# Kernel optimization log

Hardware: AMD Instinct MI355X
Metric: run time of the kernel (lower is better)

## Reference

```python
import jax, jax.numpy as jnp
import numpy as np

D = 512      # model_dim
H = 8        # num_heads
HD = D // H  # head_dim = 64
S = 196      # tokens per channel (14x14 grid)
CHANNELS = np.array([2, 4, 6, 4], dtype=np.int32)  # multiplex channels per sample


def setup_inputs() -> dict:
    key = jax.random.key(0)
    ks = jax.random.split(key, 8)
    C = int(CHANNELS.sum())  # 16
    n = lambda k, shp, s=1.0: jax.random.normal(k, shp, dtype=jnp.float32) * s
    return {
        "x_query": n(ks[0], (C, S, D)),
        "x_keyval": n(ks[1], (C, S, D)),
        "pos": n(ks[2], (C, S, D)),
        "channels": CHANNELS,
        "Wq": n(ks[3], (D, D), 0.02), "bq": jnp.zeros((D,), jnp.float32),
        "Wk": n(ks[4], (D, D), 0.02), "bk": jnp.zeros((D,), jnp.float32),
        "Wv": n(ks[5], (D, D), 0.02), "bv": jnp.zeros((D,), jnp.float32),
        "Wo": n(ks[6], (D, D), 0.02), "bo": jnp.zeros((D,), jnp.float32),
    }


def reference(x_query, x_keyval, pos, channels, Wq, bq, Wk, bk, Wv, bv, Wo, bo):
    C, S_, D_ = x_query.shape
    ch = np.asarray(channels)
    # segment id per packed token; segment i has length channels[i]*S (== cu_seq_len blocks)
    seg = np.repeat(np.arange(ch.shape[0]), ch * S_)                # [T] static
    block_mask = seg[:, None] == seg[None, :]                        # [T,T] static bool

    xq = x_query.reshape(-1, D_)   # [T,D]
    xk = x_keyval.reshape(-1, D_)
    p = pos.reshape(-1, D_)

    # positional embedding fused into Q/K before projection (query_pos/key_pos)
    q = ((xq + p) @ Wq + bq).reshape(-1, H, HD)
    k = ((xk + p) @ Wk + bk).reshape(-1, H, HD)
    v = (xk @ Wv + bv).reshape(-1, H, HD)

    scale = 1.0 / np.sqrt(HD)
    scores = jnp.einsum('qhd,khd->hqk', q, k) * scale               # [H,T,T]
    scores = jnp.where(block_mask[None], scores, jnp.float32(-1e30))
    attn = jax.nn.softmax(scores, axis=-1)
    out = jnp.einsum('hqk,khd->qhd', attn, v).reshape(-1, D_)       # [T,D]
    out = out @ Wo + bo
    return out.reshape(C, S_, D_)
```

## Files before the change

### kernel.cpp

```cpp
#include <hip/hip_runtime.h>
#include <hip/hip_bf16.h>


typedef short short8 __attribute__((ext_vector_type(8)));
typedef float f32x4 __attribute__((ext_vector_type(4)));

__device__ __forceinline__ float b2f(unsigned short u) {
    union { float f; unsigned int i; } x; x.i = ((unsigned int)u) << 16; return x.f;
}
__device__ __forceinline__ unsigned short f2b(float f) {
    union { float f; unsigned int i; } x; x.f = f;
    unsigned int r = x.i + 0x7fffu + ((x.i >> 16) & 1u);
    return (unsigned short)(r >> 16);
}

#define NE 1605632
#define WE 262144
#define GS 72

__launch_bounds__(256)
__global__ void prep(const float* __restrict__ xq, const float* __restrict__ xk,
                     const float* __restrict__ pos,
                     const float* __restrict__ W0, const float* __restrict__ W1,
                     const float* __restrict__ W2, const float* __restrict__ W3,
                     unsigned short* __restrict__ WF,
                     unsigned short* __restrict__ aqb, unsigned short* __restrict__ akb,
                     unsigned short* __restrict__ xkbb) {
    const int tid = threadIdx.x;
    if (blockIdx.z < 4) {
        if (blockIdx.x >= 128) return;
        const float* W = blockIdx.z == 0 ? W0 : blockIdx.z == 1 ? W1 : blockIdx.z == 2 ? W2 : W3;
        unsigned short* T = WF + (size_t)blockIdx.z * WE;
        const int s = blockIdx.x * 4 + (tid >> 6);
        const int f = s >> 4, t = s & 15;
        const int lane = tid & 63, quad = lane >> 4, l16 = lane & 15;
        short8 o;
        #pragma unroll
        for (int j = 0; j < 8; ++j)
            o[j] = (short)f2b(W[(size_t)(t * 32 + quad * 8 + j) * 512 + f * 16 + l16]);
        *(short8*)(T + (size_t)s * 512 + lane * 8) = o;
    } else {
        const size_t e = ((size_t)blockIdx.x * 256 + tid) * 8;
        f32x4 q0 = *(const f32x4*)(xq + e),  q1 = *(const f32x4*)(xq + e + 4);
        f32x4 k0 = *(const f32x4*)(xk + e),  k1 = *(const f32x4*)(xk + e + 4);
        f32x4 p0 = *(const f32x4*)(pos + e), p1 = *(const f32x4*)(pos + e + 4);
        short8 a, b, c;
        #pragma unroll
        for (int j = 0; j < 4; ++j) {
            a[j] = (short)f2b(q0[j] + p0[j]); a[4 + j] = (short)f2b(q1[j] + p1[j]);
            b[j] = (short)f2b(k0[j] + p0[j]); b[4 + j] = (short)f2b(k1[j] + p1[j]);
            c[j] = (short)f2b(k0[j]);         c[4 + j] = (short)f2b(k1[j]);
        }
        *(short8*)(aqb + e)  = a;
        *(short8*)(akb + e)  = b;
        *(short8*)(xkbb + e) = c;
    }
}

template <bool OUT_F32>
__device__ __forceinline__ void gemm_wave(const unsigned short* __restrict__ A,
                                          const unsigned short* __restrict__ WFw,
                                          const float* __restrict__ bias,
                                          void* __restrict__ C,
                                          int m0, int n0) {
    const int lane = threadIdx.x & 63;
    const int quad = lane >> 4, l16 = lane & 15;
    const int f0 = n0 >> 4;
    const unsigned short* Arow = A + (size_t)(m0 + l16) * 512 + quad * 8;
    const unsigned short* Bbase = WFw + (size_t)lane * 8;

    f32x4 acc[4] = {};
    #pragma unroll 4
    for (int t = 0; t < 16; ++t) {
        short8 af = *(const short8*)(Arow + t * 32);
        #pragma unroll
        for (int nt = 0; nt < 4; ++nt) {
            short8 bf = *(const short8*)(Bbase + (size_t)((f0 + nt) * 16 + t) * 512);
            acc[nt] = __builtin_amdgcn_mfma_f32_16x16x32_bf16(af, bf, acc[nt], 0, 0, 0);
        }
    }
    #pragma unroll
    for (int nt = 0; nt < 4; ++nt) {
        const int col = n0 + nt * 16 + l16;
        const float bv = bias[col];
        #pragma unroll
        for (int r = 0; r < 4; ++r) {
            const int row = m0 + quad * 4 + r;
            float cv = acc[nt][r] + bv;
            if constexpr (OUT_F32) ((float*)C)[(size_t)row * 512 + col] = cv;
            else ((unsigned short*)C)[(size_t)row * 512 + col] = f2b(cv);
        }
    }
}

__launch_bounds__(256)
__global__ void qkv_gemm(const unsigned short* __restrict__ aqb,
                         const unsigned short* __restrict__ akb,
                         const unsigned short* __restrict__ xkbb,
                         const unsigned short* __restrict__ WF,
                         const float* __restrict__ bq, const float* __restrict__ bk,
                         const float* __restrict__ bv,
                         unsigned short* __restrict__ qb, unsigned short* __restrict__ kb,
                         unsigned short* __restrict__ vb) {
    const unsigned short* A; const unsigned short* WFw; const float* bias; unsigned short* C;
    switch (blockIdx.z) {
        case 0:  A = aqb;  WFw = WF;          bias = bq; C = qb; break;
        case 1:  A = akb;  WFw = WF + WE;     bias = bk; C = kb; break;
        default: A = xkbb; WFw = WF + 2 * WE; bias = bv; C = vb; break;
    }
    gemm_wave<false>(A, WFw, bias, C, blockIdx.x * 64 + (threadIdx.x >> 6) * 16,
                     blockIdx.y * 64);
}

__launch_bounds__(256)
__global__ void out_gemm(const unsigned short* __restrict__ A,
                         const unsigned short* __restrict__ WFo,
                         const float* __restrict__ bo, float* __restrict__ out) {
    gemm_wave<true>(A, WFo, bo, out, blockIdx.x * 64 + (threadIdx.x >> 6) * 16,
                    blockIdx.y * 64);
}

__launch_bounds__(512)
__global__ void attn_seg(const unsigned short* __restrict__ q,
                         const unsigned short* __restrict__ k,
                         const unsigned short* __restrict__ v,
                         unsigned short* __restrict__ o) {
    __shared__ __align__(16) unsigned char Lds[55296];

    const int id = blockIdx.x;
    int h, off, L, qt;
    if (id < 152)      { h = id & 7; qt = id >> 3; off = 1176; L = 1176; }
    else if (id < 360) { int m = id - 152; h = m & 7; int s = m >> 3;
                         if (s < 13) { off = 392;  L = 784; qt = s; }
                         else        { off = 2352; L = 784; qt = s - 13; } }
    else               { int m = id - 360; h = m & 7; qt = m >> 3; off = 0; L = 392; }

    const int tid = threadIdx.x;
    const int wave = tid >> 6, lane = tid & 63;
    const int grp = wave >> 2, w4 = wave & 3;
    const int quad = lane >> 4, l16 = lane & 15;
    const int hb = h * 64;
    const int lastr = off + L - 1;

    unsigned short* Ks = (unsigned short*)(Lds + grp * 18432);
    unsigned short* Vt = (unsigned short*)(Lds + grp * 18432 + 9216);
    unsigned char*  Pme = Lds + 36864 + wave * 2304;

    int qrow = off + qt * 64 + w4 * 16 + l16;
    if (qrow > lastr) qrow = lastr;
    const short8 qf0 = *(const short8*)(q + (size_t)qrow * 512 + hb + quad * 8);
    const short8 qf1 = *(const short8*)(q + (size_t)qrow * 512 + hb + 32 + quad * 8);

    const int skey = lane, sd = w4 * 16;
    const int ntiles = (L + 63) >> 6;
    const int nt0 = (ntiles + 1) >> 1;

    float lsum = 0.f;
    f32x4 oacc[4] = {};

    short8 kr0, kr1, vr0, vr1;
    {
        int kk = (grp ? nt0 : 0) * 64 + skey;
        int krow = off + (kk < L ? kk : L - 1);
        kr0 = *(const short8*)(k + (size_t)krow * 512 + hb + sd);
        kr1 = *(const short8*)(k + (size_t)krow * 512 + hb + sd + 8);
        vr0 = *(const short8*)(v + (size_t)krow * 512 + hb + sd);
        vr1 = *(const short8*)(v + (size_t)krow * 512 + hb + sd + 8);
    }
    unsigned char* pwr = Pme + l16 * 144 + quad * 8;
    const unsigned char* prd = Pme + l16 * 144 + quad * 16;

    for (int i = 0; i < nt0; ++i) {
        const int tg = (grp ? nt0 : 0) + i;
        __syncthreads();
        *(short8*)(Ks + skey * GS + sd)     = kr0;
        *(short8*)(Ks + skey * GS + sd + 8) = kr1;
        #pragma unroll
        for (int j = 0; j < 8; ++j) {
            Vt[(sd + j) * GS + skey]     = (unsigned short)vr0[j];
            Vt[(sd + 8 + j) * GS + skey] = (unsigned short)vr1[j];
        }
        __syncthreads();
        if (i + 1 < nt0) {
            int kk = (tg + 1) * 64 + skey;
            int krow = off + (kk < L ? kk : L - 1);
            kr0 = *(const short8*)(k + (size_t)krow * 512 + hb + sd);
            kr1 = *(const short8*)(k + (size_t)krow * 512 + hb + sd + 8);
            vr0 = *(const short8*)(v + (size_t)krow * 512 + hb + sd);
            vr1 = *(const short8*)(v + (size_t)krow * 512 + hb + sd + 8);
        }
        f32x4 sT[4];
        #pragma unroll
        for (int g = 0; g < 4; ++g) {
            short8 kb0 = *(const short8*)(Ks + (g * 16 + l16) * GS + quad * 8);
            short8 kb1 = *(const short8*)(Ks + (g * 16 + l16) * GS + 32 + quad * 8);
            f32x4 z = {0.f, 0.f, 0.f, 0.f};
            z     = __builtin_amdgcn_mfma_f32_16x16x32_bf16(kb0, qf0, z, 0, 0, 0);
            sT[g] = __builtin_amdgcn_mfma_f32_16x16x32_bf16(kb1, qf1, z, 0, 0, 0);
        }
        const int kbase = tg * 64 + quad * 4;
        #pragma unroll
        for (int g = 0; g < 4; ++g) {
            float p[4];
            #pragma unroll
            for (int r = 0; r < 4; ++r) {
                const bool valid = (kbase + g * 16 + r) < L;
                p[r] = valid ? __expf(fminf(sT[g][r] * 0.125f, 30.f)) : 0.f;
                lsum += p[r];
            }
            #pragma unroll
            for (int i2 = 0; i2 < 2; ++i2) {
                __hip_bfloat162 t = __float22bfloat162_rn(make_float2(p[2 * i2], p[2 * i2 + 1]));
                *(unsigned int*)(pwr + g * 32 + i2 * 4) = *(unsigned int*)&t;
            }
        }
        short8 pa0 = *(const short8*)(prd);
        short8 pa1 = *(const short8*)(prd + 64);
        #pragma unroll
        for (int nt = 0; nt < 4; ++nt) {
            short8 vf0 = *(const short8*)(Vt + (nt * 16 + l16) * GS + quad * 8);
            short8 vf1 = *(const short8*)(Vt + (nt * 16 + l16) * GS + 32 + quad * 8);
            oacc[nt] = __builtin_amdgcn_mfma_f32_16x16x32_bf16(pa0, vf0, oacc[nt], 0, 0, 0);
            oacc[nt] = __builtin_amdgcn_mfma_f32_16x16x32_bf16(pa1, vf1, oacc[nt], 0, 0, 0);
        }
    }
    lsum += __shfl_xor(lsum, 16);
    lsum += __shfl_xor(lsum, 32);

    __syncthreads();
    float* Mrg = (float*)(Lds + w4 * 5120 + lane * 80);
    float* Ls  = (float*)(Lds + 20480);
    if (grp == 1) {
        #pragma unroll
        for (int nt = 0; nt < 4; ++nt) *(f32x4*)(Mrg + nt * 4) = oacc[nt];
        Ls[w4 * 64 + lane] = lsum;
    }
    __syncthreads();
    if (grp == 0) {
        lsum += Ls[w4 * 64 + lane];
        #pragma unroll
        for (int nt = 0; nt < 4; ++nt) {
            f32x4 po = *(const f32x4*)(Mrg + nt * 4);
            oacc[nt] += po;
        }
        #pragma unroll
        for (int r = 0; r < 4; ++r) {
            const float srow = __shfl(lsum, (lane & 48) + quad * 4 + r);
            const float linv = 1.0f / srow;
            const int qi = qt * 64 + w4 * 16 + quad * 4 + r;
            if (qi < L) {
                #pragma unroll
                for (int nt = 0; nt < 4; ++nt)
                    o[(size_t)(off + qi) * 512 + hb + nt * 16 + l16] = f2b(oacc[nt][r] * linv);
            }
        }
    }
}

extern "C" void kernel_launch(void* const* d_in, const int* in_sizes, int n_in,
                              void* d_out, int out_size, void* d_ws, size_t ws_size,
                              hipStream_t stream) {
    const float* xq  = (const float*)d_in[0];
    const float* xk  = (const float*)d_in[1];
    const float* pos = (const float*)d_in[2];
    const float* Wq = (const float*)d_in[4];
    const float* bq = (const float*)d_in[5];
    const float* Wk = (const float*)d_in[6];
    const float* bk = (const float*)d_in[7];
    const float* Wv = (const float*)d_in[8];
    const float* bv = (const float*)d_in[9];
    const float* Wo = (const float*)d_in[10];
    const float* bo = (const float*)d_in[11];
    float* out = (float*)d_out;

    unsigned short* ws = (unsigned short*)d_ws;
    unsigned short* qb   = ws;
    unsigned short* kb   = ws + NE;
    unsigned short* vb   = ws + (size_t)2 * NE;
    unsigned short* aqb  = ws + (size_t)3 * NE;
    unsigned short* akb  = ws + (size_t)4 * NE;
    unsigned short* xkbb = ws + (size_t)5 * NE;
    unsigned short* WF   = ws + (size_t)6 * NE;

    prep<<<dim3(784, 1, 5), 256, 0, stream>>>(xq, xk, pos, Wq, Wk, Wv, Wo,
                                              WF, aqb, akb, xkbb);
    qkv_gemm<<<dim3(49, 8, 3), 256, 0, stream>>>(aqb, akb, xkbb, WF, bq, bk, bv,
                                                 qb, kb, vb);
    attn_seg<<<dim3(416), 512, 0, stream>>>(qb, kb, vb, qb);
    out_gemm<<<dim3(49, 8), 256, 0, stream>>>(qb, WF + (size_t)3 * WE, bo, out);
}
```

Baseline: 146.3 us.

## Enlarge QKV GEMM wave tile, shrink attention LDS padding, add MFMA priority hints

```diff
diff --git a/kernel.cpp b/kernel.cpp
--- a/kernel.cpp
+++ b/kernel.cpp
@@ -16,7 +16,7 @@
 
 #define NE 1605632
 #define WE 262144
-#define GS 72
+#define GS 68
 
 __launch_bounds__(256)
 __global__ void prep(const float* __restrict__ xq, const float* __restrict__ xk,
@@ -93,6 +93,42 @@
     }
 }
 
+__device__ __forceinline__ void gemm_wave32(const unsigned short* __restrict__ A,
+                                            const unsigned short* __restrict__ WFw,
+                                            const float* __restrict__ bias,
+                                            unsigned short* __restrict__ C,
+                                            int m0, int n0) {
+    const int lane = threadIdx.x & 63;
+    const int quad = lane >> 4, l16 = lane & 15;
+    const int f0 = n0 >> 4;
+    const unsigned short* Ar0 = A + (size_t)(m0 + l16) * 512 + quad * 8;
+    const unsigned short* Bbase = WFw + (size_t)lane * 8;
+
+    f32x4 acc0[4] = {}, acc1[4] = {};
+    #pragma unroll 4
+    for (int t = 0; t < 16; ++t) {
+        short8 af0 = *(const short8*)(Ar0 + t * 32);
+        short8 af1 = *(const short8*)(Ar0 + 16 * 512 + t * 32);
+        #pragma unroll
+        for (int nt = 0; nt < 4; ++nt) {
+            short8 bf = *(const short8*)(Bbase + (size_t)((f0 + nt) * 16 + t) * 512);
+            acc0[nt] = __builtin_amdgcn_mfma_f32_16x16x32_bf16(af0, bf, acc0[nt], 0, 0, 0);
+            acc1[nt] = __builtin_amdgcn_mfma_f32_16x16x32_bf16(af1, bf, acc1[nt], 0, 0, 0);
+        }
+    }
+    #pragma unroll
+    for (int nt = 0; nt < 4; ++nt) {
+        const int col = n0 + nt * 16 + l16;
+        const float bv = bias[col];
+        #pragma unroll
+        for (int r = 0; r < 4; ++r) {
+            const int row = m0 + quad * 4 + r;
+            C[(size_t)row * 512 + col]        = f2b(acc0[nt][r] + bv);
+            C[(size_t)(row + 16) * 512 + col] = f2b(acc1[nt][r] + bv);
+        }
+    }
+}
+
 __launch_bounds__(256)
 __global__ void qkv_gemm(const unsigned short* __restrict__ aqb,
                          const unsigned short* __restrict__ akb,
@@ -108,8 +144,9 @@
         case 1:  A = akb;  WFw = WF + WE;     bias = bk; C = kb; break;
         default: A = xkbb; WFw = WF + 2 * WE; bias = bv; C = vb; break;
     }
-    gemm_wave<false>(A, WFw, bias, C, blockIdx.x * 64 + (threadIdx.x >> 6) * 16,
-                     blockIdx.y * 64);
+    const int w = threadIdx.x >> 6;
+    gemm_wave32(A, WFw, bias, C, blockIdx.x * 64 + (w & 1) * 32,
+                blockIdx.y * 128 + (w >> 1) * 64);
 }
 
 __launch_bounds__(256)
@@ -125,7 +162,7 @@
                          const unsigned short* __restrict__ k,
                          const unsigned short* __restrict__ v,
                          unsigned short* __restrict__ o) {
-    __shared__ __align__(16) unsigned char Lds[55296];
+    __shared__ __align__(16) unsigned char Lds[53248];
 
     const int id = blockIdx.x;
     int h, off, L, qt;
@@ -142,9 +179,9 @@
     const int hb = h * 64;
     const int lastr = off + L - 1;
 
-    unsigned short* Ks = (unsigned short*)(Lds + grp * 18432);
-    unsigned short* Vt = (unsigned short*)(Lds + grp * 18432 + 9216);
-    unsigned char*  Pme = Lds + 36864 + wave * 2304;
+    unsigned short* Ks = (unsigned short*)(Lds + grp * 17408);
+    unsigned short* Vt = (unsigned short*)(Lds + grp * 17408 + 8704);
+    unsigned char*  Pme = Lds + 34816 + wave * 2304;
 
     int qrow = off + qt * 64 + w4 * 16 + l16;
     if (qrow > lastr) qrow = lastr;
@@ -190,6 +227,7 @@
             vr1 = *(const short8*)(v + (size_t)krow * 512 + hb + sd + 8);
         }
         f32x4 sT[4];
+        __builtin_amdgcn_s_setprio(1);
         #pragma unroll
         for (int g = 0; g < 4; ++g) {
             short8 kb0 = *(const short8*)(Ks + (g * 16 + l16) * GS + quad * 8);
@@ -198,6 +236,7 @@
             z     = __builtin_amdgcn_mfma_f32_16x16x32_bf16(kb0, qf0, z, 0, 0, 0);
             sT[g] = __builtin_amdgcn_mfma_f32_16x16x32_bf16(kb1, qf1, z, 0, 0, 0);
         }
+        __builtin_amdgcn_s_setprio(0);
         const int kbase = tg * 64 + quad * 4;
         #pragma unroll
         for (int g = 0; g < 4; ++g) {
@@ -216,6 +255,7 @@
         }
         short8 pa0 = *(const short8*)(prd);
         short8 pa1 = *(const short8*)(prd + 64);
+        __builtin_amdgcn_s_setprio(1);
         #pragma unroll
         for (int nt = 0; nt < 4; ++nt) {
             short8 vf0 = *(const short8*)(Vt + (nt * 16 + l16) * GS + quad * 8);
@@ -223,6 +263,7 @@
             oacc[nt] = __builtin_amdgcn_mfma_f32_16x16x32_bf16(pa0, vf0, oacc[nt], 0, 0, 0);
             oacc[nt] = __builtin_amdgcn_mfma_f32_16x16x32_bf16(pa1, vf1, oacc[nt], 0, 0, 0);
         }
+        __builtin_amdgcn_s_setprio(0);
     }
     lsum += __shfl_xor(lsum, 16);
     lsum += __shfl_xor(lsum, 32);
@@ -284,7 +325,7 @@
 
     prep<<<dim3(784, 1, 5), 256, 0, stream>>>(xq, xk, pos, Wq, Wk, Wv, Wo,
                                               WF, aqb, akb, xkbb);
-    qkv_gemm<<<dim3(49, 8, 3), 256, 0, stream>>>(aqb, akb, xkbb, WF, bq, bk, bv,
+    qkv_gemm<<<dim3(49, 4, 3), 256, 0, stream>>>(aqb, akb, xkbb, WF, bq, bk, bv,
                                                  qb, kb, vb);
     attn_seg<<<dim3(416), 512, 0, stream>>>(qb, kb, vb, qb);
     out_gemm<<<dim3(49, 8), 256, 0, stream>>>(qb, WF + (size_t)3 * WE, bo, out);
```

Result: slower. 197.0 us (+34.6%).
